# Performance work log

Measured on AMD Instinct MI355X. Metric: run time of the kernel, lower is better.

The kernel has to match this reference:

```python
import jax, jax.numpy as jnp
import numpy as np

N_NODES = 100000
NNZ = 1600000
BATCH = 4
D_FEAT = 32
EPS = 1e-20


def setup_inputs() -> dict:
    key = jax.random.key(0)
    k1, k2, k3, k4 = jax.random.split(key, 4)
    x = jax.random.normal(k1, (BATCH, N_NODES, D_FEAT), dtype=jnp.float32)
    weight = jax.random.normal(k2, (NNZ,), dtype=jnp.float32)
    row = jax.random.randint(k3, (NNZ,), 0, N_NODES, dtype=jnp.int32)
    col = jax.random.randint(k4, (NNZ,), 0, N_NODES, dtype=jnp.int32)
    indices = jnp.stack([row, col], axis=0)  # [2, nnz]
    return {"x": x, "weight": weight, "indices": indices}


def reference(x, weight, indices):
    # A = sparse(indices, exp(weight), [N, N]); out = (A @ x) / (A @ ones)
    row, col = indices[0], indices[1]
    vals = jnp.exp(weight)  # [nnz]
    # messages per edge: vals_e * x[:, col_e, :], summed into row buckets
    agg = jax.vmap(
        lambda xb: jax.ops.segment_sum(xb[col] * vals[:, None], row,
                                       num_segments=N_NODES)
    )(x)  # [B, N, D]
    s = jax.ops.segment_sum(vals, row, num_segments=N_NODES)  # [N]
    return agg / (s[None, :, None] + EPS)
```

## Files before the change

kernel.cpp:

```cpp
#include <hip/hip_runtime.h>


#define N_NODES 100000
#define NNZ_E   1600000
#define BATCH   4
#define D_FEAT  32

#define RPB     64
#define NBUCK   ((N_NODES + RPB - 1) / RPB)
#define CAPR    1280
#define CAPP    1536
#define KREG    ((CAPR + 255) / 256)

#define EPB     8192
#define PBLK    ((NNZ_E + EPB - 1) / EPB)
#define TBLK    2048


__global__ __launch_bounds__(1024) void prep_fused(
    const float* __restrict__ x, unsigned int* __restrict__ xt,
    const int4* __restrict__ row4, const int4* __restrict__ col4,
    const float4* __restrict__ w4,
    int* __restrict__ gcur, unsigned long long* __restrict__ recs) {
    const int t = threadIdx.x;

    if (blockIdx.x >= PBLK) {
        const int totalT  = N_NODES * 64;
        const int strideT = TBLK * 1024;
        for (int i = (blockIdx.x - PBLK) * 1024 + t; i < totalT; i += strideT) {
            int n = i >> 6, q = i & 63;
            int b = q >> 4, d = (q & 15) * 2;
            const float* src = x + ((size_t)b * N_NODES + n) * 32 + d;
            unsigned int a  = __float_as_uint(src[0]);
            unsigned int bu = __float_as_uint(src[1]);
            a  = (a  + 0x7fffu + ((a  >> 16) & 1u)) >> 16;
            bu = (bu + 0x7fffu + ((bu >> 16) & 1u)) & 0xffff0000u;
            xt[i] = bu | a;
        }
        return;
    }

    __shared__ int hist[NBUCK];
    __shared__ int gbase[NBUCK];
    __shared__ int lofs[NBUCK];

    for (int b = t; b < NBUCK; b += 1024) hist[b] = 0;
    __syncthreads();

    const int base4 = blockIdx.x * (EPB / 4);
#pragma unroll
    for (int rnd = 0; rnd < EPB / 4 / 1024; ++rnd) {
        int i4 = base4 + rnd * 1024 + t;
        if (i4 < NNZ_E / 4) {
            int4 r = row4[i4];
            atomicAdd(&hist[r.x >> 6], 1);
            atomicAdd(&hist[r.y >> 6], 1);
            atomicAdd(&hist[r.z >> 6], 1);
            atomicAdd(&hist[r.w >> 6], 1);
        }
    }
    __syncthreads();
    for (int b = t; b < NBUCK; b += 1024) {
        int c = hist[b];
        lofs[b] = 0;
        if (c > 0) gbase[b] = atomicAdd(&gcur[b], c);
    }
    __syncthreads();
#pragma unroll
    for (int rnd = 0; rnd < EPB / 4 / 1024; ++rnd) {
        int i4 = base4 + rnd * 1024 + t;
        if (i4 < NNZ_E / 4) {
            int4   r = row4[i4];
            int4   c = col4[i4];
            float4 w = w4[i4];
            int   rr[4] = {r.x, r.y, r.z, r.w};
            int   cc[4] = {c.x, c.y, c.z, c.w};
            float vv[4] = {__expf(w.x), __expf(w.y), __expf(w.z), __expf(w.w)};
#pragma unroll
            for (int k = 0; k < 4; ++k) {
                int b    = rr[k] >> 6;
                int slot = atomicAdd(&lofs[b], 1);
                int pos  = gbase[b] + slot;
                if (pos < CAPR) {
                    unsigned int key =
                        ((unsigned int)(rr[k] & (RPB - 1)) << 17) | (unsigned int)cc[k];
                    recs[(size_t)b * CAPR + pos] =
                        ((unsigned long long)__float_as_uint(vv[k]) << 32) | key;
                }
            }
        }
    }
}


#define CONSUME(RC, P)                                           \
    {                                                            \
        float v = __uint_as_float((unsigned int)((RC) >> 32));   \
        sv   += v;                                               \
        acc0 += v * __uint_as_float((P).x << 16);                \
        acc1 += v * __uint_as_float((P).x & 0xffff0000u);        \
        acc2 += v * __uint_as_float((P).y << 16);                \
        acc3 += v * __uint_as_float((P).y & 0xffff0000u);        \
        acc4 += v * __uint_as_float((P).z << 16);                \
        acc5 += v * __uint_as_float((P).z & 0xffff0000u);        \
        acc6 += v * __uint_as_float((P).w << 16);                \
        acc7 += v * __uint_as_float((P).w & 0xffff0000u);        \
    }

__global__ __launch_bounds__(256) void bucket_sort_aggregate(
    const unsigned int* __restrict__ xt,
    const int* __restrict__ gcur,
    const unsigned long long* __restrict__ recs_g,
    float* __restrict__ out) {
    __shared__ unsigned long long srec[CAPP];
    __shared__ int cnt[RPB];
    __shared__ int poff[RPB];
    __shared__ int cur[RPB];

    const int t = threadIdx.x;
    const int bucket = blockIdx.x;
    int count = gcur[bucket];
    if (count > CAPR) count = CAPR;
    const unsigned long long* recs = recs_g + (size_t)bucket * CAPR;

    for (int i = t; i < CAPP; i += 256) srec[i] = 0ull;
    if (t < RPB) cnt[t] = 0;

    unsigned long long rl[KREG];
#pragma unroll
    for (int k = 0; k < KREG; ++k) {
        int i = t + k * 256;
        rl[k] = (i < count) ? recs[i] : 0ull;
    }
    __syncthreads();

#pragma unroll
    for (int k = 0; k < KREG; ++k)
        if (t + k * 256 < count)
            atomicAdd(&cnt[((unsigned int)rl[k]) >> 17], 1);
    __syncthreads();

    if (t < RPB) poff[t] = (cnt[t] + 3) & ~3;
    __syncthreads();
    for (int o = 1; o < RPB; o <<= 1) {
        int v = 0;
        if (t < RPB && t >= o) v = poff[t - o];
        __syncthreads();
        if (t < RPB) poff[t] += v;
        __syncthreads();
    }
    if (t < RPB) cur[t] = poff[t] - ((cnt[t] + 3) & ~3);
    __syncthreads();

#pragma unroll
    for (int k = 0; k < KREG; ++k)
        if (t + k * 256 < count) {
            int pos = atomicAdd(&cur[((unsigned int)rl[k]) >> 17], 1);
            srec[pos] = rl[k];
        }
    __syncthreads();

    const int wave = t >> 6;
    const int lane = t & 63;
    const int eg   = lane >> 4;
    const int s16  = lane & 15;
    const uint4* xr = (const uint4*)xt;

    for (int rr = wave * 16; rr < wave * 16 + 16; ++rr) {
        int node = bucket * RPB + rr;
        if (node >= N_NODES) break;
        int np   = (cnt[rr] + 3) & ~3;
        int base = poff[rr] - np;

        float acc0 = 0.f, acc1 = 0.f, acc2 = 0.f, acc3 = 0.f;
        float acc4 = 0.f, acc5 = 0.f, acc6 = 0.f, acc7 = 0.f, sv = 0.f;

        int j = 0;
        for (; j + 16 <= np; j += 16) {
            unsigned long long r0 = srec[base + j + eg];
            unsigned long long r1 = srec[base + j + 4 + eg];
            unsigned long long r2 = srec[base + j + 8 + eg];
            unsigned long long r3 = srec[base + j + 12 + eg];
            uint4 p0 = xr[(((size_t)((unsigned int)r0 & 0x1ffffu)) << 4) + s16];
            uint4 p1 = xr[(((size_t)((unsigned int)r1 & 0x1ffffu)) << 4) + s16];
            uint4 p2 = xr[(((size_t)((unsigned int)r2 & 0x1ffffu)) << 4) + s16];
            uint4 p3 = xr[(((size_t)((unsigned int)r3 & 0x1ffffu)) << 4) + s16];
            CONSUME(r0, p0);
            CONSUME(r1, p1);
            CONSUME(r2, p2);
            CONSUME(r3, p3);
        }
        for (; j < np; j += 4) {
            unsigned long long r0 = srec[base + j + eg];
            uint4 p0 = xr[(((size_t)((unsigned int)r0 & 0x1ffffu)) << 4) + s16];
            CONSUME(r0, p0);
        }

        acc0 += __shfl_xor(acc0, 16); acc0 += __shfl_xor(acc0, 32);
        acc1 += __shfl_xor(acc1, 16); acc1 += __shfl_xor(acc1, 32);
        acc2 += __shfl_xor(acc2, 16); acc2 += __shfl_xor(acc2, 32);
        acc3 += __shfl_xor(acc3, 16); acc3 += __shfl_xor(acc3, 32);
        acc4 += __shfl_xor(acc4, 16); acc4 += __shfl_xor(acc4, 32);
        acc5 += __shfl_xor(acc5, 16); acc5 += __shfl_xor(acc5, 32);
        acc6 += __shfl_xor(acc6, 16); acc6 += __shfl_xor(acc6, 32);
        acc7 += __shfl_xor(acc7, 16); acc7 += __shfl_xor(acc7, 32);
        sv   += __shfl_xor(sv,   16); sv   += __shfl_xor(sv,   32);

        float inv = 1.0f / (sv + 1e-20f);
        if (eg < 2) {
            int f4 = s16 * 2 + eg;
            int b  = f4 >> 3;
            float4 o;
            o.x = (eg ? acc4 : acc0) * inv;
            o.y = (eg ? acc5 : acc1) * inv;
            o.z = (eg ? acc6 : acc2) * inv;
            o.w = (eg ? acc7 : acc3) * inv;
            ((float4*)out)[((size_t)b * N_NODES + node) * 8 + (f4 & 7)] = o;
        }
    }
}


__global__ __launch_bounds__(256) void edge_scatter(
    const float* __restrict__ x, const float* __restrict__ weight,
    const int* __restrict__ row, const int* __restrict__ col,
    float* __restrict__ out, float* __restrict__ s) {
    int tid = blockIdx.x * blockDim.x + threadIdx.x;
    int e = tid >> 3, sub = tid & 7;
    if (e >= NNZ_E) return;
    int r = row[e], c = col[e];
    float v = __expf(weight[e]);
    if (sub == 0) atomicAdd(&s[r], v);
    const float4* x4 = (const float4*)x;
#pragma unroll
    for (int b = 0; b < BATCH; ++b) {
        float4 xv = x4[(size_t)(b * N_NODES + c) * 8 + sub];
        float* o = out + (size_t)(b * N_NODES + r) * 32 + sub * 4;
        atomicAdd(o + 0, v * xv.x); atomicAdd(o + 1, v * xv.y);
        atomicAdd(o + 2, v * xv.z); atomicAdd(o + 3, v * xv.w);
    }
}

__global__ __launch_bounds__(256) void divide_kernel(
    float* __restrict__ out, const float* __restrict__ s) {
    int i = blockIdx.x * blockDim.x + threadIdx.x;
    const int total4 = BATCH * N_NODES * (D_FEAT / 4);
    if (i >= total4) return;
    int node = (i >> 3) % N_NODES;
    float inv = 1.0f / (s[node] + 1e-20f);
    float4* o4 = (float4*)out;
    float4 v = o4[i];
    v.x *= inv; v.y *= inv; v.z *= inv; v.w *= inv;
    o4[i] = v;
}


extern "C" void kernel_launch(void* const* d_in, const int* in_sizes, int n_in,
                              void* d_out, int out_size, void* d_ws, size_t ws_size,
                              hipStream_t stream) {
    const float* x      = (const float*)d_in[0];
    const float* weight = (const float*)d_in[1];
    const int*   idx    = (const int*)d_in[2];
    const int*   row    = idx;
    const int*   col    = idx + NNZ_E;
    float* out = (float*)d_out;

    const size_t GCUR_BYTES = ((size_t)NBUCK * 4 + 4095) & ~(size_t)4095;
    const size_t REC_BYTES  = (size_t)NBUCK * CAPR * 8;
    const size_t XT_BYTES   = (size_t)N_NODES * 64 * 4;
    const size_t REQUIRED   = GCUR_BYTES + REC_BYTES + XT_BYTES;

    if (ws_size >= REQUIRED) {
        char* ws = (char*)d_ws;
        int* gcur = (int*)ws;
        unsigned long long* recs = (unsigned long long*)(ws + GCUR_BYTES);
        unsigned int* xt = (unsigned int*)(ws + GCUR_BYTES + REC_BYTES);

        hipMemsetAsync(gcur, 0, (size_t)NBUCK * 4, stream);
        prep_fused<<<PBLK + TBLK, 1024, 0, stream>>>(
            x, xt, (const int4*)row, (const int4*)col, (const float4*)weight,
            gcur, recs);
        bucket_sort_aggregate<<<NBUCK, 256, 0, stream>>>(xt, gcur, recs, out);
    } else {
        float* s = (float*)d_ws;
        hipMemsetAsync(out, 0, (size_t)out_size * sizeof(float), stream);
        hipMemsetAsync(s, 0, (size_t)N_NODES * sizeof(float), stream);
        long long threads_total = (long long)NNZ_E * 8;
        int grid = (int)((threads_total + 255) / 256);
        edge_scatter<<<grid, 256, 0, stream>>>(x, weight, row, col, out, s);
        int total4 = BATCH * N_NODES * (D_FEAT / 4);
        divide_kernel<<<(total4 + 255) / 256, 256, 0, stream>>>(out, s);
    }
}
```

Measured before the change: 111.1 us.

## Fuse prep and bucket aggregation into one cooperative kernel with grid sync

Adds a cooperative mega-kernel that does the bf16 transpose of x, the per-bucket edge histogram and scatter, and then, after a grid-wide sync, the per-bucket local sort and aggregation. The goal is to remove the second kernel launch and the gap between the two stages. The trade-off is that each block now scatters only 1024 edges, so many more blocks do global cursor atomics than before, and the grid barrier has its own cost. The old two-kernel path stays as a fallback if the cooperative launch fails.

```diff
diff --git a/kernel.cpp b/kernel.cpp
--- a/kernel.cpp
+++ b/kernel.cpp
@@ -1,4 +1,7 @@
 #include <hip/hip_runtime.h>
+#include <hip/hip_cooperative_groups.h>
+
+namespace cg = cooperative_groups;
 
 
 #define N_NODES 100000
@@ -17,81 +20,13 @@
 #define TBLK    2048
 
 
-__global__ __launch_bounds__(1024) void prep_fused(
-    const float* __restrict__ x, unsigned int* __restrict__ xt,
-    const int4* __restrict__ row4, const int4* __restrict__ col4,
-    const float4* __restrict__ w4,
-    int* __restrict__ gcur, unsigned long long* __restrict__ recs) {
-    const int t = threadIdx.x;
-
-    if (blockIdx.x >= PBLK) {
-        const int totalT  = N_NODES * 64;
-        const int strideT = TBLK * 1024;
-        for (int i = (blockIdx.x - PBLK) * 1024 + t; i < totalT; i += strideT) {
-            int n = i >> 6, q = i & 63;
-            int b = q >> 4, d = (q & 15) * 2;
-            const float* src = x + ((size_t)b * N_NODES + n) * 32 + d;
-            unsigned int a  = __float_as_uint(src[0]);
-            unsigned int bu = __float_as_uint(src[1]);
-            a  = (a  + 0x7fffu + ((a  >> 16) & 1u)) >> 16;
-            bu = (bu + 0x7fffu + ((bu >> 16) & 1u)) & 0xffff0000u;
-            xt[i] = bu | a;
-        }
-        return;
-    }
-
-    __shared__ int hist[NBUCK];
-    __shared__ int gbase[NBUCK];
-    __shared__ int lofs[NBUCK];
-
-    for (int b = t; b < NBUCK; b += 1024) hist[b] = 0;
-    __syncthreads();
-
-    const int base4 = blockIdx.x * (EPB / 4);
-#pragma unroll
-    for (int rnd = 0; rnd < EPB / 4 / 1024; ++rnd) {
-        int i4 = base4 + rnd * 1024 + t;
-        if (i4 < NNZ_E / 4) {
-            int4 r = row4[i4];
-            atomicAdd(&hist[r.x >> 6], 1);
-            atomicAdd(&hist[r.y >> 6], 1);
-            atomicAdd(&hist[r.z >> 6], 1);
-            atomicAdd(&hist[r.w >> 6], 1);
-        }
-    }
-    __syncthreads();
-    for (int b = t; b < NBUCK; b += 1024) {
-        int c = hist[b];
-        lofs[b] = 0;
-        if (c > 0) gbase[b] = atomicAdd(&gcur[b], c);
-    }
-    __syncthreads();
-#pragma unroll
-    for (int rnd = 0; rnd < EPB / 4 / 1024; ++rnd) {
-        int i4 = base4 + rnd * 1024 + t;
-        if (i4 < NNZ_E / 4) {
-            int4   r = row4[i4];
-            int4   c = col4[i4];
-            float4 w = w4[i4];
-            int   rr[4] = {r.x, r.y, r.z, r.w};
-            int   cc[4] = {c.x, c.y, c.z, c.w};
-            float vv[4] = {__expf(w.x), __expf(w.y), __expf(w.z), __expf(w.w)};
-#pragma unroll
-            for (int k = 0; k < 4; ++k) {
-                int b    = rr[k] >> 6;
-                int slot = atomicAdd(&lofs[b], 1);
-                int pos  = gbase[b] + slot;
-                if (pos < CAPR) {
-                    unsigned int key =
-                        ((unsigned int)(rr[k] & (RPB - 1)) << 17) | (unsigned int)cc[k];
-                    recs[(size_t)b * CAPR + pos] =
-                        ((unsigned long long)__float_as_uint(vv[k]) << 32) | key;
-                }
-            }
-        }
-    }
-}
-
+__device__ __forceinline__ unsigned int pack_bf16(float lo, float hi) {
+    unsigned int a = __float_as_uint(lo);
+    unsigned int b = __float_as_uint(hi);
+    a = (a + 0x7fffu + ((a >> 16) & 1u)) >> 16;
+    b = (b + 0x7fffu + ((b >> 16) & 1u)) & 0xffff0000u;
+    return b | a;
+}
 
 #define CONSUME(RC, P)                                           \
     {                                                            \
@@ -106,6 +41,244 @@
         acc6 += v * __uint_as_float((P).w << 16);                \
         acc7 += v * __uint_as_float((P).w & 0xffff0000u);        \
     }
+
+
+__global__ __launch_bounds__(256, 7) void mega_kernel(
+    const float* __restrict__ x, unsigned int* __restrict__ xt,
+    const int* __restrict__ row, const int* __restrict__ col,
+    const float* __restrict__ weight,
+    int* __restrict__ gcur, unsigned long long* __restrict__ recs,
+    float* __restrict__ out) {
+    __shared__ union {
+        struct { int hist[NBUCK]; int cursor[NBUCK]; } a;
+        struct { unsigned long long srec[CAPP];
+                 int cnt[RPB]; int poff[RPB]; int cur[RPB]; } b;
+    } sh;
+
+    const int t = threadIdx.x;
+    const int g = blockIdx.x * 256 + t;
+
+    const int totalT = N_NODES * 64;
+    for (int i = g; i < totalT; i += NBUCK * 256) {
+        int n = i >> 6, q = i & 63;
+        int b = q >> 4, d = (q & 15) * 2;
+        const float* src = x + ((size_t)b * N_NODES + n) * 32 + d;
+        xt[i] = pack_bf16(src[0], src[1]);
+    }
+
+    for (int i = t; i < NBUCK; i += 256) sh.a.hist[i] = 0;
+    __syncthreads();
+
+    const bool valid = g < NNZ_E / 4;
+    int4 r4, c4;
+    float4 w4;
+    if (valid) {
+        r4 = ((const int4*)row)[g];
+        c4 = ((const int4*)col)[g];
+        w4 = ((const float4*)weight)[g];
+        atomicAdd(&sh.a.hist[r4.x >> 6], 1);
+        atomicAdd(&sh.a.hist[r4.y >> 6], 1);
+        atomicAdd(&sh.a.hist[r4.z >> 6], 1);
+        atomicAdd(&sh.a.hist[r4.w >> 6], 1);
+    }
+    __syncthreads();
+    for (int b = t; b < NBUCK; b += 256) {
+        int h = sh.a.hist[b];
+        if (h > 0) sh.a.cursor[b] = atomicAdd(&gcur[b], h);
+    }
+    __syncthreads();
+    if (valid) {
+        int   rr[4] = {r4.x, r4.y, r4.z, r4.w};
+        int   cc[4] = {c4.x, c4.y, c4.z, c4.w};
+        float vv[4] = {__expf(w4.x), __expf(w4.y), __expf(w4.z), __expf(w4.w)};
+#pragma unroll
+        for (int k = 0; k < 4; ++k) {
+            int b    = rr[k] >> 6;
+            int pos  = atomicAdd(&sh.a.cursor[b], 1);
+            if (pos < CAPR) {
+                unsigned int key =
+                    ((unsigned int)(rr[k] & (RPB - 1)) << 17) | (unsigned int)cc[k];
+                recs[(size_t)b * CAPR + pos] =
+                    ((unsigned long long)__float_as_uint(vv[k]) << 32) | key;
+            }
+        }
+    }
+
+    cg::this_grid().sync();
+
+    const int bucket = blockIdx.x;
+    int count = gcur[bucket];
+    if (count > CAPR) count = CAPR;
+    const unsigned long long* brecs = recs + (size_t)bucket * CAPR;
+
+    for (int i = t; i < CAPP; i += 256) sh.b.srec[i] = 0ull;
+    if (t < RPB) sh.b.cnt[t] = 0;
+
+    unsigned long long rl[KREG];
+#pragma unroll
+    for (int k = 0; k < KREG; ++k) {
+        int i = t + k * 256;
+        rl[k] = (i < count) ? brecs[i] : 0ull;
+    }
+    __syncthreads();
+
+#pragma unroll
+    for (int k = 0; k < KREG; ++k)
+        if (t + k * 256 < count)
+            atomicAdd(&sh.b.cnt[((unsigned int)rl[k]) >> 17], 1);
+    __syncthreads();
+
+    if (t < RPB) sh.b.poff[t] = (sh.b.cnt[t] + 3) & ~3;
+    __syncthreads();
+    for (int o = 1; o < RPB; o <<= 1) {
+        int v = 0;
+        if (t < RPB && t >= o) v = sh.b.poff[t - o];
+        __syncthreads();
+        if (t < RPB) sh.b.poff[t] += v;
+        __syncthreads();
+    }
+    if (t < RPB) sh.b.cur[t] = sh.b.poff[t] - ((sh.b.cnt[t] + 3) & ~3);
+    __syncthreads();
+
+#pragma unroll
+    for (int k = 0; k < KREG; ++k)
+        if (t + k * 256 < count) {
+            int pos = atomicAdd(&sh.b.cur[((unsigned int)rl[k]) >> 17], 1);
+            sh.b.srec[pos] = rl[k];
+        }
+    __syncthreads();
+
+    const int wave = t >> 6;
+    const int lane = t & 63;
+    const int eg   = lane >> 4;
+    const int s16  = lane & 15;
+    const uint4* xr = (const uint4*)xt;
+
+    for (int rr = wave * 16; rr < wave * 16 + 16; ++rr) {
+        int node = bucket * RPB + rr;
+        if (node >= N_NODES) break;
+        int np   = (sh.b.cnt[rr] + 3) & ~3;
+        int base = sh.b.poff[rr] - np;
+
+        float acc0 = 0.f, acc1 = 0.f, acc2 = 0.f, acc3 = 0.f;
+        float acc4 = 0.f, acc5 = 0.f, acc6 = 0.f, acc7 = 0.f, sv = 0.f;
+
+        int j = 0;
+        for (; j + 16 <= np; j += 16) {
+            unsigned long long r0 = sh.b.srec[base + j + eg];
+            unsigned long long r1 = sh.b.srec[base + j + 4 + eg];
+            unsigned long long r2 = sh.b.srec[base + j + 8 + eg];
+            unsigned long long r3 = sh.b.srec[base + j + 12 + eg];
+            uint4 p0 = xr[(((size_t)((unsigned int)r0 & 0x1ffffu)) << 4) + s16];
+            uint4 p1 = xr[(((size_t)((unsigned int)r1 & 0x1ffffu)) << 4) + s16];
+            uint4 p2 = xr[(((size_t)((unsigned int)r2 & 0x1ffffu)) << 4) + s16];
+            uint4 p3 = xr[(((size_t)((unsigned int)r3 & 0x1ffffu)) << 4) + s16];
+            CONSUME(r0, p0);
+            CONSUME(r1, p1);
+            CONSUME(r2, p2);
+            CONSUME(r3, p3);
+        }
+        for (; j < np; j += 4) {
+            unsigned long long r0 = sh.b.srec[base + j + eg];
+            uint4 p0 = xr[(((size_t)((unsigned int)r0 & 0x1ffffu)) << 4) + s16];
+            CONSUME(r0, p0);
+        }
+
+        acc0 += __shfl_xor(acc0, 16); acc0 += __shfl_xor(acc0, 32);
+        acc1 += __shfl_xor(acc1, 16); acc1 += __shfl_xor(acc1, 32);
+        acc2 += __shfl_xor(acc2, 16); acc2 += __shfl_xor(acc2, 32);
+        acc3 += __shfl_xor(acc3, 16); acc3 += __shfl_xor(acc3, 32);
+        acc4 += __shfl_xor(acc4, 16); acc4 += __shfl_xor(acc4, 32);
+        acc5 += __shfl_xor(acc5, 16); acc5 += __shfl_xor(acc5, 32);
+        acc6 += __shfl_xor(acc6, 16); acc6 += __shfl_xor(acc6, 32);
+        acc7 += __shfl_xor(acc7, 16); acc7 += __shfl_xor(acc7, 32);
+        sv   += __shfl_xor(sv,   16); sv   += __shfl_xor(sv,   32);
+
+        float inv = 1.0f / (sv + 1e-20f);
+        if (eg < 2) {
+            int f4 = s16 * 2 + eg;
+            int b  = f4 >> 3;
+            float4 o;
+            o.x = (eg ? acc4 : acc0) * inv;
+            o.y = (eg ? acc5 : acc1) * inv;
+            o.z = (eg ? acc6 : acc2) * inv;
+            o.w = (eg ? acc7 : acc3) * inv;
+            ((float4*)out)[((size_t)b * N_NODES + node) * 8 + (f4 & 7)] = o;
+        }
+    }
+}
+
+
+__global__ __launch_bounds__(1024) void prep_fused(
+    const float* __restrict__ x, unsigned int* __restrict__ xt,
+    const int4* __restrict__ row4, const int4* __restrict__ col4,
+    const float4* __restrict__ w4,
+    int* __restrict__ gcur, unsigned long long* __restrict__ recs) {
+    const int t = threadIdx.x;
+
+    if (blockIdx.x >= PBLK) {
+        const int totalT  = N_NODES * 64;
+        const int strideT = TBLK * 1024;
+        for (int i = (blockIdx.x - PBLK) * 1024 + t; i < totalT; i += strideT) {
+            int n = i >> 6, q = i & 63;
+            int b = q >> 4, d = (q & 15) * 2;
+            const float* src = x + ((size_t)b * N_NODES + n) * 32 + d;
+            xt[i] = pack_bf16(src[0], src[1]);
+        }
+        return;
+    }
+
+    __shared__ int hist[NBUCK];
+    __shared__ int gbase[NBUCK];
+    __shared__ int lofs[NBUCK];
+
+    for (int b = t; b < NBUCK; b += 1024) hist[b] = 0;
+    __syncthreads();
+
+    const int base4 = blockIdx.x * (EPB / 4);
+#pragma unroll
+    for (int rnd = 0; rnd < EPB / 4 / 1024; ++rnd) {
+        int i4 = base4 + rnd * 1024 + t;
+        if (i4 < NNZ_E / 4) {
+            int4 r = row4[i4];
+            atomicAdd(&hist[r.x >> 6], 1);
+            atomicAdd(&hist[r.y >> 6], 1);
+            atomicAdd(&hist[r.z >> 6], 1);
+            atomicAdd(&hist[r.w >> 6], 1);
+        }
+    }
+    __syncthreads();
+    for (int b = t; b < NBUCK; b += 1024) {
+        int c = hist[b];
+        lofs[b] = 0;
+        if (c > 0) gbase[b] = atomicAdd(&gcur[b], c);
+    }
+    __syncthreads();
+#pragma unroll
+    for (int rnd = 0; rnd < EPB / 4 / 1024; ++rnd) {
+        int i4 = base4 + rnd * 1024 + t;
+        if (i4 < NNZ_E / 4) {
+            int4   r = row4[i4];
+            int4   c = col4[i4];
+            float4 w = w4[i4];
+            int   rr[4] = {r.x, r.y, r.z, r.w};
+            int   cc[4] = {c.x, c.y, c.z, c.w};
+            float vv[4] = {__expf(w.x), __expf(w.y), __expf(w.z), __expf(w.w)};
+#pragma unroll
+            for (int k = 0; k < 4; ++k) {
+                int b    = rr[k] >> 6;
+                int slot = atomicAdd(&lofs[b], 1);
+                int pos  = gbase[b] + slot;
+                if (pos < CAPR) {
+                    unsigned int key =
+                        ((unsigned int)(rr[k] & (RPB - 1)) << 17) | (unsigned int)cc[k];
+                    recs[(size_t)b * CAPR + pos] =
+                        ((unsigned long long)__float_as_uint(vv[k]) << 32) | key;
+                }
+            }
+        }
+    }
+}
 
 __global__ __launch_bounds__(256) void bucket_sort_aggregate(
     const unsigned int* __restrict__ xt,
@@ -277,10 +450,19 @@
         unsigned int* xt = (unsigned int*)(ws + GCUR_BYTES + REC_BYTES);
 
         hipMemsetAsync(gcur, 0, (size_t)NBUCK * 4, stream);
-        prep_fused<<<PBLK + TBLK, 1024, 0, stream>>>(
-            x, xt, (const int4*)row, (const int4*)col, (const float4*)weight,
-            gcur, recs);
-        bucket_sort_aggregate<<<NBUCK, 256, 0, stream>>>(xt, gcur, recs, out);
+
+        void* args[] = {(void*)&x, (void*)&xt, (void*)&row, (void*)&col,
+                        (void*)&weight, (void*)&gcur, (void*)&recs, (void*)&out};
+        hipError_t err = hipLaunchCooperativeKernel(
+            (const void*)mega_kernel, dim3(NBUCK), dim3(256), args, 0, stream);
+
+        if (err != hipSuccess) {
+            (void)hipGetLastError();
+            prep_fused<<<PBLK + TBLK, 1024, 0, stream>>>(
+                x, xt, (const int4*)row, (const int4*)col, (const float4*)weight,
+                gcur, recs);
+            bucket_sort_aggregate<<<NBUCK, 256, 0, stream>>>(xt, gcur, recs, out);
+        }
     } else {
         float* s = (float*)d_ws;
         hipMemsetAsync(out, 0, (size_t)out_size * sizeof(float), stream);
```

Result: slower. 318.5 us, median of 2 (+186.6%).
